# Optimization experiments

Measured on AMD Instinct MI355X. Metric: run time of the kernel, lower is better.

The kernel has to match this reference:

```python
import jax, jax.numpy as jnp
import numpy as np
from functools import reduce

N = 16          # total qubits
N_SQC = 4       # shadow-circuit qubits
BATCH = 512
DIM = 2 ** N    # 65536
CX = jnp.complex64


def multi_kron(mats):
    return reduce(jnp.kron, mats)


def ry(t):
    c = jnp.cos(t / 2).astype(CX)
    s = jnp.sin(t / 2).astype(CX)
    return jnp.stack([jnp.stack([c, -s]), jnp.stack([s, c])])


def rz(t):
    e = jnp.exp(-0.5j * t.astype(CX))
    z = jnp.zeros((), CX)
    return jnp.stack([jnp.stack([e, z]), jnp.stack([z, jnp.conj(e)])])


def yzy_layer(params, n):
    # per qubit i: apply Ry(p[3i]), Rz(p[3i+1]), Ry(p[3i+2]) -> u_i = Ry@Rz@Ry
    us = [ry(params[3 * i + 2]) @ rz(params[3 * i + 1]) @ ry(params[3 * i])
          for i in range(n)]
    return multi_kron(us)


def cnot(n, c, t):
    I = jnp.eye(2, dtype=CX)
    X = jnp.array([[0, 1], [1, 0]], dtype=CX)
    P0 = jnp.array([[1, 0], [0, 0]], dtype=CX)
    P1 = jnp.array([[0, 0], [0, 1]], dtype=CX)
    ops0 = [I] * n; ops0[c] = P0
    ops1 = [I] * n; ops1[c] = P1; ops1[t] = X
    return multi_kron(ops0) + multi_kron(ops1)


def ring_of_cnot(n):
    U = jnp.eye(2 ** n, dtype=CX)
    for i in range(n):  # CNOT(i, (i+1)%n) applied in order
        U = cnot(n, i, (i + 1) % n) @ U
    return U


def build_circuit(weight, n):
    # BasicEntangleLayer(repeat=2): [YZYLayer, ring_of_cnot] x 2, then final YZYLayer
    repeat = 2
    U = jnp.eye(2 ** n, dtype=CX)
    ring = ring_of_cnot(n)
    for r in range(repeat):
        U = yzy_layer(weight[3 * n * r:3 * n * (r + 1)], n) @ U
        U = ring @ U
    U = yzy_layer(weight[3 * n * repeat:3 * n * (repeat + 1)], n) @ U
    return U


def setup_inputs() -> dict:
    key = jax.random.key(0)
    k1, k2 = jax.random.split(key)
    vector_batch = jax.random.normal(k1, (BATCH, DIM), dtype=jnp.float32)
    weight = jax.random.uniform(k2, (9 * N_SQC,), dtype=jnp.float32,
                                minval=0.0, maxval=2.0 * np.pi)
    return {"vector_batch": vector_batch, "weight": weight}


def reference(vector_batch, weight):
    # row-wise L2 normalization + amplitude encoding (pad to 2**N), cast complex
    norm = jnp.sqrt(jnp.sum(vector_batch * vector_batch, axis=1, keepdims=True))
    state = (vector_batch / norm).astype(CX)
    state = jnp.pad(state, ((0, 0), (0, DIM - state.shape[1])))  # (B, 2^N)

    U = build_circuit(weight, N_SQC)                 # (2^n_sqc, 2^n_sqc)
    X = jnp.array([[0, 1], [1, 0]], dtype=CX)
    M = multi_kron([X] * N_SQC)                      # PauliX^{(x)n_sqc}
    T = U.conj().T @ M @ U                           # effective observable

    m = 2 ** N_SQC
    outs = []
    for start in range(N - N_SQC + 1):
        left = 2 ** start
        right = DIM // (left * m)
        # trace(rho * (I (x) T (x) I)) == <s| I (x) T (x) I |s>
        s = state.reshape(BATCH, left, m, right)
        y = jnp.einsum('ij,bajd->baid', T, s)
        o = jnp.einsum('baid,baid->b', jnp.conj(s), y).real
        outs.append(o)
    return jnp.stack(outs, axis=1).astype(jnp.float32)  # (B, N - n_sqc + 1)
```

## Files before the change

kernel.cpp:

```cpp
#include <hip/hip_runtime.h>
#include <math.h>


typedef _Float16 f16x8 __attribute__((ext_vector_type(8)));
typedef float f32x4 __attribute__((ext_vector_type(4)));
typedef float f32x16 __attribute__((ext_vector_type(16)));
#define MFMAH(a, b, c) __builtin_amdgcn_mfma_f32_16x16x32_f16((a), (b), (c), 0, 0, 0)
#define MFMA32(a, b, c) __builtin_amdgcn_mfma_f32_32x32x16_f16((a), (b), (c), 0, 0, 0)

union H4 { _Float16 h[4]; uint2 q; };
union Frag { _Float16 h[8]; f16x8 v; uint2 q[2]; unsigned int w[4]; };

__device__ __forceinline__ int swz(int g) { return g ^ (g >> 5); }

__device__ __forceinline__ float wave_sum(float x) {
    #pragma unroll
    for (int off = 32; off > 0; off >>= 1) x += __shfl_down(x, off, 64);
    return x;
}

using c2 = float2;
__device__ __forceinline__ c2 cmul(c2 a, c2 b) {
    return make_float2(a.x * b.x - a.y * b.y, a.x * b.y + a.y * b.x);
}
__device__ __forceinline__ c2 cadd(c2 a, c2 b) { return make_float2(a.x + b.x, a.y + b.y); }

__device__ __forceinline__ c2 kelem(const c2 u[4][2][2], int i, int j) {
    c2 p = cmul(u[0][(i >> 3) & 1][(j >> 3) & 1], u[1][(i >> 2) & 1][(j >> 2) & 1]);
    p = cmul(p, u[2][(i >> 1) & 1][(j >> 1) & 1]);
    p = cmul(p, u[3][i & 1][j & 1]);
    return p;
}
__device__ __forceinline__ int fperm(int x) {
    int b3 = (x >> 3) & 1, b2 = (x >> 2) & 1, b1 = (x >> 1) & 1, b0 = x & 1;
    b2 ^= b3; b1 ^= b2; b0 ^= b1; b3 ^= b0;
    return (b3 << 3) | (b2 << 2) | (b1 << 1) | b0;
}

__global__ __launch_bounds__(256) void setup_kernel(const float* __restrict__ weight,
                                                    float* __restrict__ ws) {
    __shared__ c2 ush[3][4][2][2];
    __shared__ c2 A[256], B[256];
    const int t = threadIdx.x;

    if (t < 12) {
        const int r = t / 4, q = t % 4;
        const float a = weight[12 * r + 3 * q + 0];
        const float b = weight[12 * r + 3 * q + 1];
        const float c = weight[12 * r + 3 * q + 2];
        const float ca = cosf(0.5f * a), sa = sinf(0.5f * a);
        const float cc = cosf(0.5f * c), sc = sinf(0.5f * c);
        const c2 e = make_float2(cosf(0.5f * b), -sinf(0.5f * b));
        const c2 eb = make_float2(e.x, -e.y);
        ush[r][q][0][0] = make_float2(cc * ca * e.x - sc * sa * eb.x, cc * ca * e.y - sc * sa * eb.y);
        ush[r][q][0][1] = make_float2(-cc * sa * e.x - sc * ca * eb.x, -cc * sa * e.y - sc * ca * eb.y);
        ush[r][q][1][0] = make_float2(sc * ca * e.x + cc * sa * eb.x, sc * ca * e.y + cc * sa * eb.y);
        ush[r][q][1][1] = make_float2(-sc * sa * e.x + cc * ca * eb.x, -sc * sa * e.y + cc * ca * eb.y);
    }
    __syncthreads();

    const int i = t >> 4, j = t & 15;
    A[t] = kelem(ush[0], i, j);
    __syncthreads();
    B[fperm(i) * 16 + j] = A[t];
    __syncthreads();
    {
        c2 acc = make_float2(0.f, 0.f);
        #pragma unroll
        for (int k = 0; k < 16; ++k) acc = cadd(acc, cmul(kelem(ush[1], i, k), B[k * 16 + j]));
        __syncthreads();
        A[t] = acc;
    }
    __syncthreads();
    B[fperm(i) * 16 + j] = A[t];
    __syncthreads();
    {
        c2 acc = make_float2(0.f, 0.f);
        #pragma unroll
        for (int k = 0; k < 16; ++k) acc = cadd(acc, cmul(kelem(ush[2], i, k), B[k * 16 + j]));
        __syncthreads();
        A[t] = acc;
    }
    __syncthreads();
    {
        float wr = 0.f;
        #pragma unroll
        for (int k = 0; k < 16; ++k) {
            const c2 a = A[k * 16 + i];
            const c2 b = A[(k ^ 15) * 16 + j];
            wr += a.x * b.x + a.y * b.y;
        }
        ws[t] = wr;
    }
    for (int z = t; z < 512 * 14; z += 256) ws[256 + z] = 0.f;
}


__device__ __forceinline__ void contract16(const float* __restrict__ Wl, const f32x4& acc,
                                           int i, int h, int l, float* dst) {
    const float4 wr = *(const float4*)&Wl[(i << 4) + (h << 2)];
    float q = wr.x * acc[0] + wr.y * acc[1] + wr.z * acc[2] + wr.w * acc[3];
    q = wave_sum(q);
    if (l == 0) atomicAdd(dst, q);
}

template <int S>
__device__ __forceinline__ void pair_unit(const unsigned short* __restrict__ sh16,
                                          const float* __restrict__ Wl,
                                          int l, float* accrow) {
    const int Jp = l & 31, h2 = l >> 5;
    f32x16 acc = {0.f, 0.f, 0.f, 0.f, 0.f, 0.f, 0.f, 0.f,
                  0.f, 0.f, 0.f, 0.f, 0.f, 0.f, 0.f, 0.f};
    #pragma unroll
    for (int cc = 0; cc < 16; ++cc) {
        int e0;
        if (S == 3)      e0 = (Jp << 8) + (cc << 4) + (h2 << 3);
        else if (S == 5) e0 = ((cc >> 2) << 11) + (Jp << 6) + ((cc & 3) << 4) + (h2 << 3);
        else             e0 = (cc << 9) + (Jp << 4) + (h2 << 3);
        const f16x8 f = *(const f16x8*)&sh16[swz(e0 >> 3) << 3];
        acc = MFMA32(f, f, acc);
    }
    float qa = 0.f, qb = 0.f;
    #pragma unroll
    for (int r2 = 0; r2 < 8; ++r2) {
        const int r = 2 * r2;
        const int J = (r & 3) + 8 * (r >> 2) + 4 * h2;
        const float w = Wl[((J >> 1) << 4) + (Jp >> 1)];
        qa += w * ((Jp & 1) ? acc[r + 1] : acc[r]);
    }
    #pragma unroll
    for (int r = 0; r < 8; ++r) {
        const int J = (r & 3) + 8 * (r >> 2) + 4 * h2;
        const float w = Wl[((J & 15) << 4) + (Jp & 15)];
        qb += w * ((Jp & 16) ? acc[r + 8] : acc[r]);
    }
    qa = wave_sum(qa);
    qb = wave_sum(qb);
    if (l == 0) { atomicAdd(&accrow[S], qa); atomicAdd(&accrow[S + 1], qb); }
}

__device__ __forceinline__ void unit9(const unsigned short* __restrict__ sh16,
                                      const float* __restrict__ Wl,
                                      int i, int h, int l, float* accrow) {
    f32x4 acc = {0.f, 0.f, 0.f, 0.f};
    #pragma unroll
    for (int cc = 0; cc < 16; ++cc) {
        const int e0 = ((4 * cc + h) << 7) + (i << 3);
        const f16x8 f = *(const f16x8*)&sh16[swz(e0 >> 3) << 3];
        acc = MFMAH(f, f, acc);
    }
    contract16(Wl, acc, i, h, l, &accrow[9]);
}

__device__ __forceinline__ void unit10(const unsigned short* __restrict__ sh16,
                                       const float* __restrict__ Wl,
                                       int i, int h, int l, int c0, int c1, float* accrow) {
    f32x4 acc = {0.f, 0.f, 0.f, 0.f};
    #pragma unroll
    for (int cc = c0; cc < c1; ++cc) {
        const int a0 = 8 * cc + 2 * h;
        const int ea = a0 * 64 + 4 * i;
        const int eb = ea + 64;
        Frag fr;
        fr.q[0] = *(const uint2*)&sh16[(swz(ea >> 3) << 3) + (ea & 7)];
        fr.q[1] = *(const uint2*)&sh16[(swz(eb >> 3) << 3) + (eb & 7)];
        acc = MFMAH(fr.v, fr.v, acc);
    }
    contract16(Wl, acc, i, h, l, &accrow[10]);
}

__device__ __forceinline__ void unit11(const unsigned short* __restrict__ sh16,
                                       const float* __restrict__ Wl,
                                       int i, int h, int l, int c0, int c1, float* accrow) {
    f32x4 acc = {0.f, 0.f, 0.f, 0.f};
    #pragma unroll
    for (int cc = c0; cc < c1; ++cc) {
        Frag fr;
        #pragma unroll
        for (int p = 0; p < 4; ++p) {
            const int ap = 16 * cc + 4 * h + p;
            const int e = ap * 32 + 2 * i;
            fr.w[p] = *(const unsigned int*)&sh16[(swz(e >> 3) << 3) + (e & 7)];
        }
        acc = MFMAH(fr.v, fr.v, acc);
    }
    contract16(Wl, acc, i, h, l, &accrow[11]);
}

__global__ __launch_bounds__(256, 5) void main_kernel(const float* __restrict__ v,
                                                      const float* __restrict__ ws,
                                                      float* __restrict__ accg) {
    __shared__ unsigned short sh16[8192];
    __shared__ float Wl[256];
    const int t = threadIdx.x;
    const int l = t & 63, wv = t >> 6;
    const int i = l & 15, h = l >> 4;
    Wl[t] = ws[t];

    const int bi = blockIdx.x;
    const int g = bi >> 3;
    const int unit = g & 15;
    const int row = ((g >> 4) << 3) | (bi & 7);
    float* accrow = &accg[row * 14];

    if (unit < 8) {
        const int seg = unit;
        const float4* b4 = (const float4*)(v + ((size_t)row << 16) + (seg << 13));

        float ss = 0.f;
        #pragma unroll
        for (int m = 0; m < 8; ++m) {
            const float4 d = b4[m * 256 + t];
            ss = fmaf(d.x, d.x, ss); ss = fmaf(d.y, d.y, ss);
            ss = fmaf(d.z, d.z, ss); ss = fmaf(d.w, d.w, ss);
            H4 p;
            p.h[0] = (_Float16)d.x; p.h[1] = (_Float16)d.y;
            p.h[2] = (_Float16)d.z; p.h[3] = (_Float16)d.w;
            const int e0 = (m * 256 + t) * 4;
            const int idx = (swz(e0 >> 3) << 3) + (e0 & 7);
            *(uint2*)&sh16[idx] = p.q;
        }
        {
            const float s2 = wave_sum(ss);
            if (l == 0) atomicAdd(&accrow[13], s2);
        }
        __syncthreads();

        if (wv == 0) {
            pair_unit<3>(sh16, Wl, l, accrow);
            unit10(sh16, Wl, i, h, l, 0, 8, accrow);
        } else if (wv == 1) {
            pair_unit<5>(sh16, Wl, l, accrow);
            unit10(sh16, Wl, i, h, l, 8, 16, accrow);
        } else if (wv == 2) {
            pair_unit<7>(sh16, Wl, l, accrow);
            unit11(sh16, Wl, i, h, l, 0, 8, accrow);
        } else {
            unit9(sh16, Wl, i, h, l, accrow);
            unit11(sh16, Wl, i, h, l, 8, 16, accrow);
        }
    } else {
        const int c0 = (unit - 8) << 6;
        const float* bp = v + ((size_t)row << 16) + c0 + l;

        #pragma unroll
        for (int m = 0; m < 8; ++m) {
            const int u0 = 32 * wv + 4 * m;
            H4 p;
            p.h[0] = (_Float16)bp[(u0 + 0) * 512];
            p.h[1] = (_Float16)bp[(u0 + 1) * 512];
            p.h[2] = (_Float16)bp[(u0 + 2) * 512];
            p.h[3] = (_Float16)bp[(u0 + 3) * 512];
            *(uint2*)&sh16[l * 128 + (u0 ^ (8 * (l & 15)))] = p.q;
        }
        __syncthreads();

        if (wv == 0) {
            f32x4 acc = {0.f, 0.f, 0.f, 0.f};
            #pragma unroll
            for (int cc = 0; cc < 16; ++cc) {
                const int cl = 4 * cc + h;
                const f16x8 f = *(const f16x8*)&sh16[cl * 128 + ((8 * i) ^ (8 * (cl & 15)))];
                acc = MFMAH(f, f, acc);
            }
            contract16(Wl, acc, i, h, l, &accrow[0]);
        } else if (wv == 1) {
            {
                f32x4 acc = {0.f, 0.f, 0.f, 0.f};
                #pragma unroll
                for (int cc = 0; cc < 16; ++cc) {
                    const int cl = 4 * cc + h;
                    const int k = 8 * (cl & 15);
                    Frag fr;
                    fr.q[0] = *(const uint2*)&sh16[cl * 128 + ((4 * i) ^ k)];
                    fr.q[1] = *(const uint2*)&sh16[cl * 128 + ((64 + 4 * i) ^ k)];
                    acc = MFMAH(fr.v, fr.v, acc);
                }
                contract16(Wl, acc, i, h, l, &accrow[1]);
            }
            {
                f32x4 acc = {0.f, 0.f, 0.f, 0.f};
                #pragma unroll
                for (int cc = 12; cc < 16; ++cc) {
                    const int cl = 4 * cc + h;
                    const int k = 8 * (cl & 15);
                    Frag fr;
                    #pragma unroll
                    for (int p = 0; p < 4; ++p)
                        fr.w[p] = *(const unsigned int*)&sh16[cl * 128 + ((2 * i + 32 * p) ^ k)];
                    acc = MFMAH(fr.v, fr.v, acc);
                }
                contract16(Wl, acc, i, h, l, &accrow[2]);
            }
        } else if (wv == 2) {
            f32x4 acc = {0.f, 0.f, 0.f, 0.f};
            #pragma unroll
            for (int cc = 0; cc < 12; ++cc) {
                const int cl = 4 * cc + h;
                const int k = 8 * (cl & 15);
                Frag fr;
                #pragma unroll
                for (int p = 0; p < 4; ++p)
                    fr.w[p] = *(const unsigned int*)&sh16[cl * 128 + ((2 * i + 32 * p) ^ k)];
                acc = MFMAH(fr.v, fr.v, acc);
            }
            contract16(Wl, acc, i, h, l, &accrow[2]);
        } else {
            f32x4 acc = {0.f, 0.f, 0.f, 0.f};
            #pragma unroll
            for (int cc = 0; cc < 16; ++cc) {
                const int k0 = 32 * cc + 8 * h;
                const int cg = k0 >> 7, u0 = k0 & 127;
                const int col = 16 * cg + i;
                const f16x8 f = *(const f16x8*)&sh16[col * 128 + (u0 ^ (8 * i))];
                acc = MFMAH(f, f, acc);
            }
            contract16(Wl, acc, i, h, l, &accrow[12]);
        }
    }
}

__global__ __launch_bounds__(256) void finalize_kernel(const float* __restrict__ acc,
                                                       float* __restrict__ out) {
    const int idx = blockIdx.x * 256 + threadIdx.x;
    if (idx < 512 * 13) {
        const int row = idx / 13, s = idx % 13;
        out[idx] = acc[row * 14 + s] / acc[row * 14 + 13];
    }
}

extern "C" void kernel_launch(void* const* d_in, const int* in_sizes, int n_in,
                              void* d_out, int out_size, void* d_ws, size_t ws_size,
                              hipStream_t stream) {
    const float* vb = (const float*)d_in[0];
    const float* wt = (const float*)d_in[1];
    float* out = (float*)d_out;
    float* ws = (float*)d_ws;
    float* acc = ws + 256;

    setup_kernel<<<1, 256, 0, stream>>>(wt, ws);
    main_kernel<<<8192, 256, 0, stream>>>(vb, ws, acc);
    finalize_kernel<<<26, 256, 0, stream>>>(acc, out);
}
```

Measured before the change: 194.9 us.

## Keep whole rows in 128KB LDS per 1024-thread block, read input once

Replaces the 8192-block scheme, which reads each row twice (contiguous segments plus a strided column pass), with 256 blocks of 1024 threads. Each block stages a full 64K-element row as fp16 in 128KB of dynamic LDS across 8 chunks. The local-qubit windows are computed per chunk, and the cross-chunk windows (0-2) run once the row is fully resident. Global loads are software-prefetched one chunk ahead to overlap with the MFMA work. This cuts global traffic to a single coalesced read but leaves only one block per CU, with barriers every chunk and a 256-block grid that may underfill the GPU.

```diff
diff --git a/kernel.cpp b/kernel.cpp
--- a/kernel.cpp
+++ b/kernel.cpp
@@ -8,7 +8,6 @@
 #define MFMAH(a, b, c) __builtin_amdgcn_mfma_f32_16x16x32_f16((a), (b), (c), 0, 0, 0)
 #define MFMA32(a, b, c) __builtin_amdgcn_mfma_f32_32x32x16_f16((a), (b), (c), 0, 0, 0)
 
-union H4 { _Float16 h[4]; uint2 q; };
 union Frag { _Float16 h[8]; f16x8 v; uint2 q[2]; unsigned int w[4]; };
 
 __device__ __forceinline__ int swz(int g) { return g ^ (g >> 5); }
@@ -104,55 +103,59 @@
     if (l == 0) atomicAdd(dst, q);
 }
 
+__device__ __forceinline__ void pair_contract(const f32x16& acc, const float* __restrict__ Wl,
+                                              int Jp, int h2, int l,
+                                              float* dqa, float* dqb) {
+    float qa = 0.f, qb = 0.f;
+    #pragma unroll
+    for (int r2 = 0; r2 < 8; ++r2) {
+        const int r = 2 * r2;
+        const int J = (r & 3) + 8 * (r >> 2) + 4 * h2;
+        qa += Wl[((J >> 1) << 4) + (Jp >> 1)] * ((Jp & 1) ? acc[r + 1] : acc[r]);
+    }
+    #pragma unroll
+    for (int r = 0; r < 8; ++r) {
+        const int J = (r & 3) + 8 * (r >> 2) + 4 * h2;
+        qb += Wl[((J & 15) << 4) + (Jp & 15)] * ((Jp & 16) ? acc[r + 8] : acc[r]);
+    }
+    qa = wave_sum(qa);
+    qb = wave_sum(qb);
+    if (l == 0) { atomicAdd(dqa, qa); atomicAdd(dqb, qb); }
+}
+
 template <int S>
-__device__ __forceinline__ void pair_unit(const unsigned short* __restrict__ sh16,
+__device__ __forceinline__ void pair_unit(const unsigned short* __restrict__ sh,
                                           const float* __restrict__ Wl,
-                                          int l, float* accrow) {
+                                          int l, int c0, int c1, float* accrow) {
     const int Jp = l & 31, h2 = l >> 5;
     f32x16 acc = {0.f, 0.f, 0.f, 0.f, 0.f, 0.f, 0.f, 0.f,
                   0.f, 0.f, 0.f, 0.f, 0.f, 0.f, 0.f, 0.f};
     #pragma unroll
-    for (int cc = 0; cc < 16; ++cc) {
+    for (int cc = c0; cc < c1; ++cc) {
         int e0;
         if (S == 3)      e0 = (Jp << 8) + (cc << 4) + (h2 << 3);
         else if (S == 5) e0 = ((cc >> 2) << 11) + (Jp << 6) + ((cc & 3) << 4) + (h2 << 3);
         else             e0 = (cc << 9) + (Jp << 4) + (h2 << 3);
-        const f16x8 f = *(const f16x8*)&sh16[swz(e0 >> 3) << 3];
+        const f16x8 f = *(const f16x8*)&sh[swz(e0 >> 3) << 3];
         acc = MFMA32(f, f, acc);
     }
-    float qa = 0.f, qb = 0.f;
-    #pragma unroll
-    for (int r2 = 0; r2 < 8; ++r2) {
-        const int r = 2 * r2;
-        const int J = (r & 3) + 8 * (r >> 2) + 4 * h2;
-        const float w = Wl[((J >> 1) << 4) + (Jp >> 1)];
-        qa += w * ((Jp & 1) ? acc[r + 1] : acc[r]);
-    }
-    #pragma unroll
-    for (int r = 0; r < 8; ++r) {
-        const int J = (r & 3) + 8 * (r >> 2) + 4 * h2;
-        const float w = Wl[((J & 15) << 4) + (Jp & 15)];
-        qb += w * ((Jp & 16) ? acc[r + 8] : acc[r]);
-    }
-    qa = wave_sum(qa);
-    qb = wave_sum(qb);
-    if (l == 0) { atomicAdd(&accrow[S], qa); atomicAdd(&accrow[S + 1], qb); }
-}
-
-__device__ __forceinline__ void unit9(const unsigned short* __restrict__ sh16,
+    pair_contract(acc, Wl, Jp, h2, l, &accrow[S], &accrow[S + 1]);
+}
+
+__device__ __forceinline__ void unit9(const unsigned short* __restrict__ sh,
                                       const float* __restrict__ Wl,
-                                      int i, int h, int l, float* accrow) {
+                                      int i, int h, int l, int c0, int c1, float* accrow) {
     f32x4 acc = {0.f, 0.f, 0.f, 0.f};
     #pragma unroll
-    for (int cc = 0; cc < 16; ++cc) {
+    for (int cc = c0; cc < c1; ++cc) {
         const int e0 = ((4 * cc + h) << 7) + (i << 3);
-        const f16x8 f = *(const f16x8*)&sh16[swz(e0 >> 3) << 3];
+        const f16x8 f = *(const f16x8*)&sh[swz(e0 >> 3) << 3];
         acc = MFMAH(f, f, acc);
     }
     contract16(Wl, acc, i, h, l, &accrow[9]);
 }
 
-__device__ __forceinline__ void unit10(const unsigned short* __restrict__ sh16,
+__device__ __forceinline__ void unit10(const unsigned short* __restrict__ sh,
                                        const float* __restrict__ Wl,
                                        int i, int h, int l, int c0, int c1, float* accrow) {
     f32x4 acc = {0.f, 0.f, 0.f, 0.f};
@@ -162,14 +165,14 @@
         const int ea = a0 * 64 + 4 * i;
         const int eb = ea + 64;
         Frag fr;
-        fr.q[0] = *(const uint2*)&sh16[(swz(ea >> 3) << 3) + (ea & 7)];
-        fr.q[1] = *(const uint2*)&sh16[(swz(eb >> 3) << 3) + (eb & 7)];
+        fr.q[0] = *(const uint2*)&sh[(swz(ea >> 3) << 3) + (ea & 7)];
+        fr.q[1] = *(const uint2*)&sh[(swz(eb >> 3) << 3) + (eb & 7)];
         acc = MFMAH(fr.v, fr.v, acc);
     }
     contract16(Wl, acc, i, h, l, &accrow[10]);
 }
 
-__device__ __forceinline__ void unit11(const unsigned short* __restrict__ sh16,
+__device__ __forceinline__ void unit11(const unsigned short* __restrict__ sh,
                                        const float* __restrict__ Wl,
                                        int i, int h, int l, int c0, int c1, float* accrow) {
     f32x4 acc = {0.f, 0.f, 0.f, 0.f};
@@ -180,143 +183,117 @@
         for (int p = 0; p < 4; ++p) {
             const int ap = 16 * cc + 4 * h + p;
             const int e = ap * 32 + 2 * i;
-            fr.w[p] = *(const unsigned int*)&sh16[(swz(e >> 3) << 3) + (e & 7)];
+            fr.w[p] = *(const unsigned int*)&sh[(swz(e >> 3) << 3) + (e & 7)];
         }
         acc = MFMAH(fr.v, fr.v, acc);
     }
     contract16(Wl, acc, i, h, l, &accrow[11]);
 }
 
-__global__ __launch_bounds__(256, 5) void main_kernel(const float* __restrict__ v,
-                                                      const float* __restrict__ ws,
-                                                      float* __restrict__ accg) {
-    __shared__ unsigned short sh16[8192];
+__device__ __forceinline__ void unitW0(const unsigned short* __restrict__ sh,
+                                       const float* __restrict__ Wl,
+                                       int i, int h, int l, int c0, int c1, float* accrow) {
+    f32x4 acc = {0.f, 0.f, 0.f, 0.f};
+    #pragma unroll
+    for (int cc = c0; cc < c1; ++cc) {
+        Frag fr;
+        #pragma unroll
+        for (int p = 0; p < 8; ++p) {
+            const int e = i + ((cc * 32 + h * 8 + p) << 4);
+            fr.h[p] = *(const _Float16*)&sh[(swz(e >> 3) << 3) + (e & 7)];
+        }
+        acc = MFMAH(fr.v, fr.v, acc);
+    }
+    contract16(Wl, acc, i, h, l, &accrow[12]);
+}
+
+__global__ __launch_bounds__(1024) void main_kernel(const float* __restrict__ v,
+                                                    const float* __restrict__ ws,
+                                                    float* __restrict__ accg) {
+    extern __shared__ __align__(16) unsigned short sh16[];
     __shared__ float Wl[256];
     const int t = threadIdx.x;
     const int l = t & 63, wv = t >> 6;
     const int i = l & 15, h = l >> 4;
-    Wl[t] = ws[t];
-
-    const int bi = blockIdx.x;
-    const int g = bi >> 3;
-    const int unit = g & 15;
-    const int row = ((g >> 4) << 3) | (bi & 7);
-    float* accrow = &accg[row * 14];
-
-    if (unit < 8) {
-        const int seg = unit;
-        const float4* b4 = (const float4*)(v + ((size_t)row << 16) + (seg << 13));
-
-        float ss = 0.f;
-        #pragma unroll
-        for (int m = 0; m < 8; ++m) {
-            const float4 d = b4[m * 256 + t];
-            ss = fmaf(d.x, d.x, ss); ss = fmaf(d.y, d.y, ss);
-            ss = fmaf(d.z, d.z, ss); ss = fmaf(d.w, d.w, ss);
-            H4 p;
-            p.h[0] = (_Float16)d.x; p.h[1] = (_Float16)d.y;
-            p.h[2] = (_Float16)d.z; p.h[3] = (_Float16)d.w;
-            const int e0 = (m * 256 + t) * 4;
-            const int idx = (swz(e0 >> 3) << 3) + (e0 & 7);
-            *(uint2*)&sh16[idx] = p.q;
-        }
-        {
-            const float s2 = wave_sum(ss);
-            if (l == 0) atomicAdd(&accrow[13], s2);
-        }
+    const int J = l & 31, h2 = l >> 5;
+    if (t < 256) Wl[t] = ws[t];
+
+    const float4* __restrict__ base = (const float4*)(v + ((size_t)blockIdx.x << 17));
+    float* accrow = accg + (size_t)(2 * blockIdx.x) * 14;
+
+    float4 a0 = base[2 * t], a1 = base[2 * t + 1];
+    float ss = 0.f;
+
+    for (int k = 0; k < 16; ++k) {
+        float4 b0, b1;
+        const bool more = (k < 15);
+        if (more) {
+            b0 = base[(k + 1) * 2048 + 2 * t];
+            b1 = base[(k + 1) * 2048 + 2 * t + 1];
+        }
+
+        ss = fmaf(a0.x, a0.x, ss); ss = fmaf(a0.y, a0.y, ss);
+        ss = fmaf(a0.z, a0.z, ss); ss = fmaf(a0.w, a0.w, ss);
+        ss = fmaf(a1.x, a1.x, ss); ss = fmaf(a1.y, a1.y, ss);
+        ss = fmaf(a1.z, a1.z, ss); ss = fmaf(a1.w, a1.w, ss);
+        Frag fr;
+        fr.h[0] = (_Float16)a0.x; fr.h[1] = (_Float16)a0.y;
+        fr.h[2] = (_Float16)a0.z; fr.h[3] = (_Float16)a0.w;
+        fr.h[4] = (_Float16)a1.x; fr.h[5] = (_Float16)a1.y;
+        fr.h[6] = (_Float16)a1.z; fr.h[7] = (_Float16)a1.w;
+        const int c = k & 7;
+        *(f16x8*)&sh16[(c << 13) + (swz(t) << 3)] = fr.v;
         __syncthreads();
 
-        if (wv == 0) {
-            pair_unit<3>(sh16, Wl, l, accrow);
-            unit10(sh16, Wl, i, h, l, 0, 8, accrow);
-        } else if (wv == 1) {
-            pair_unit<5>(sh16, Wl, l, accrow);
-            unit10(sh16, Wl, i, h, l, 8, 16, accrow);
-        } else if (wv == 2) {
-            pair_unit<7>(sh16, Wl, l, accrow);
-            unit11(sh16, Wl, i, h, l, 0, 8, accrow);
-        } else {
-            unit9(sh16, Wl, i, h, l, accrow);
-            unit11(sh16, Wl, i, h, l, 8, 16, accrow);
-        }
-    } else {
-        const int c0 = (unit - 8) << 6;
-        const float* bp = v + ((size_t)row << 16) + c0 + l;
-
-        #pragma unroll
-        for (int m = 0; m < 8; ++m) {
-            const int u0 = 32 * wv + 4 * m;
-            H4 p;
-            p.h[0] = (_Float16)bp[(u0 + 0) * 512];
-            p.h[1] = (_Float16)bp[(u0 + 1) * 512];
-            p.h[2] = (_Float16)bp[(u0 + 2) * 512];
-            p.h[3] = (_Float16)bp[(u0 + 3) * 512];
-            *(uint2*)&sh16[l * 128 + (u0 ^ (8 * (l & 15)))] = p.q;
-        }
-        __syncthreads();
-
-        if (wv == 0) {
-            f32x4 acc = {0.f, 0.f, 0.f, 0.f};
-            #pragma unroll
-            for (int cc = 0; cc < 16; ++cc) {
-                const int cl = 4 * cc + h;
-                const f16x8 f = *(const f16x8*)&sh16[cl * 128 + ((8 * i) ^ (8 * (cl & 15)))];
-                acc = MFMAH(f, f, acc);
-            }
-            contract16(Wl, acc, i, h, l, &accrow[0]);
-        } else if (wv == 1) {
+        const unsigned short* sh = &sh16[c << 13];
+        const int half = (wv & 1) << 3;
+        if (wv < 2)       pair_unit<3>(sh, Wl, l, half, half + 8, accrow);
+        else if (wv < 4)  pair_unit<5>(sh, Wl, l, half, half + 8, accrow);
+        else if (wv < 6)  pair_unit<7>(sh, Wl, l, half, half + 8, accrow);
+        else if (wv < 8)  unit9 (sh, Wl, i, h, l, half, half + 8, accrow);
+        else if (wv < 10) unit10(sh, Wl, i, h, l, half, half + 8, accrow);
+        else if (wv < 12) unit11(sh, Wl, i, h, l, half, half + 8, accrow);
+        else {
+            const int q0 = (wv - 12) << 2;
+            unitW0(sh, Wl, i, h, l, q0, q0 + 4, accrow);
+        }
+
+        if (c == 7) {
             {
                 f32x4 acc = {0.f, 0.f, 0.f, 0.f};
                 #pragma unroll
-                for (int cc = 0; cc < 16; ++cc) {
-                    const int cl = 4 * cc + h;
-                    const int k = 8 * (cl & 15);
-                    Frag fr;
-                    fr.q[0] = *(const uint2*)&sh16[cl * 128 + ((4 * i) ^ k)];
-                    fr.q[1] = *(const uint2*)&sh16[cl * 128 + ((64 + 4 * i) ^ k)];
-                    acc = MFMAH(fr.v, fr.v, acc);
+                for (int j = 0; j < 8; ++j) {
+                    const int cc = (wv << 3) + j;
+                    const int e = (i << 12) + cc * 32 + h * 8;
+                    const f16x8 f = *(const f16x8*)
+                        &sh16[((e >> 13) << 13) + (swz((e & 8191) >> 3) << 3)];
+                    acc = MFMAH(f, f, acc);
                 }
-                contract16(Wl, acc, i, h, l, &accrow[1]);
+                contract16(Wl, acc, i, h, l, &accrow[0]);
             }
             {
-                f32x4 acc = {0.f, 0.f, 0.f, 0.f};
+                f32x16 acc = {0.f, 0.f, 0.f, 0.f, 0.f, 0.f, 0.f, 0.f,
+                              0.f, 0.f, 0.f, 0.f, 0.f, 0.f, 0.f, 0.f};
                 #pragma unroll
-                for (int cc = 12; cc < 16; ++cc) {
-                    const int cl = 4 * cc + h;
-                    const int k = 8 * (cl & 15);
-                    Frag fr;
-                    #pragma unroll
-                    for (int p = 0; p < 4; ++p)
-                        fr.w[p] = *(const unsigned int*)&sh16[cl * 128 + ((2 * i + 32 * p) ^ k)];
-                    acc = MFMAH(fr.v, fr.v, acc);
+                for (int j = 0; j < 8; ++j) {
+                    const int cc = (wv << 3) + j;
+                    const int kg = cc * 16 + h2 * 8;
+                    const int e = (J << 10) + (kg & 1023) + ((kg >> 10) << 15);
+                    const f16x8 f = *(const f16x8*)
+                        &sh16[((e >> 13) << 13) + (swz((e & 8191) >> 3) << 3)];
+                    acc = MFMA32(f, f, acc);
                 }
-                contract16(Wl, acc, i, h, l, &accrow[2]);
+                pair_contract(acc, Wl, J, h2, l, &accrow[1], &accrow[2]);
             }
-        } else if (wv == 2) {
-            f32x4 acc = {0.f, 0.f, 0.f, 0.f};
-            #pragma unroll
-            for (int cc = 0; cc < 12; ++cc) {
-                const int cl = 4 * cc + h;
-                const int k = 8 * (cl & 15);
-                Frag fr;
-                #pragma unroll
-                for (int p = 0; p < 4; ++p)
-                    fr.w[p] = *(const unsigned int*)&sh16[cl * 128 + ((2 * i + 32 * p) ^ k)];
-                acc = MFMAH(fr.v, fr.v, acc);
+            {
+                const float s2 = wave_sum(ss);
+                if (l == 0) atomicAdd(&accrow[13], s2);
+                ss = 0.f;
             }
-            contract16(Wl, acc, i, h, l, &accrow[2]);
-        } else {
-            f32x4 acc = {0.f, 0.f, 0.f, 0.f};
-            #pragma unroll
-            for (int cc = 0; cc < 16; ++cc) {
-                const int k0 = 32 * cc + 8 * h;
-                const int cg = k0 >> 7, u0 = k0 & 127;
-                const int col = 16 * cg + i;
-                const f16x8 f = *(const f16x8*)&sh16[col * 128 + (u0 ^ (8 * i))];
-                acc = MFMAH(f, f, acc);
-            }
-            contract16(Wl, acc, i, h, l, &accrow[12]);
-        }
+            __syncthreads();
+            accrow += 14;
+        }
+        if (more) { a0 = b0; a1 = b1; }
     }
 }
 
@@ -338,7 +315,14 @@
     float* ws = (float*)d_ws;
     float* acc = ws + 256;
 
+    static bool attr_set = false;
+    if (!attr_set) {
+        (void)hipFuncSetAttribute((const void*)main_kernel,
+                                  hipFuncAttributeMaxDynamicSharedMemorySize, 131072);
+        attr_set = true;
+    }
+
     setup_kernel<<<1, 256, 0, stream>>>(wt, ws);
-    main_kernel<<<8192, 256, 0, stream>>>(vb, ws, acc);
+    main_kernel<<<256, 1024, 131072, stream>>>(vb, ws, acc);
     finalize_kernel<<<26, 256, 0, stream>>>(acc, out);
 }
```

Result: slower. 253.9 us (+30.3%).
